# Kernel tuning notes

Measured on AMD Instinct MI355X. Metric: run time of the kernel, lower is better.

Reference implementation:

```python
import math
import jax, jax.numpy as jnp
import numpy as np

H = 1024          # hidden size
NH = 16           # num attention heads
HD = H // NH      # head dim = 64
MAXPOS = 1024
HYP_W = 0.5


def setup_inputs() -> dict:
    key = jax.random.key(0)
    ks = jax.random.split(key, 9)
    B, S = 4, 1024
    scale = 1.0 / math.sqrt(H)
    return {
        "hidden_states": jax.random.normal(ks[0], (B, S, H), jnp.float32),
        "attention_mask": jnp.zeros((B, 1, 1, S), jnp.float32),
        "hyperbolic_attention_scores": jax.random.normal(ks[1], (B, S, S), jnp.float32),
        "Wq": jax.random.normal(ks[2], (H, H), jnp.float32) * scale,
        "bq": jnp.zeros((H,), jnp.float32),
        "Wk": jax.random.normal(ks[3], (H, H), jnp.float32) * scale,
        "bk": jnp.zeros((H,), jnp.float32),
        "Wv": jax.random.normal(ks[4], (H, H), jnp.float32) * scale,
        "bv": jnp.zeros((H,), jnp.float32),
        "dist_emb": jax.random.normal(ks[5], (2 * MAXPOS - 1, HD), jnp.float32) * 0.02,
    }


def reference(hidden_states, attention_mask, hyperbolic_attention_scores,
              Wq, bq, Wk, bk, Wv, bv, dist_emb):
    B, S, _ = hidden_states.shape

    def split_heads(x):  # [B,S,H] -> [B,NH,S,HD]
        return x.reshape(B, S, NH, HD).transpose(0, 2, 1, 3)

    q = split_heads(hidden_states @ Wq + bq)
    k = split_heads(hidden_states @ Wk + bk)
    v = split_heads(hidden_states @ Wv + bv)

    # raw scores [B,NH,Sq,Sk]
    scores = jnp.einsum("bhqd,bhkd->bhqk", q, k)

    # relative_key_query position bias
    distance = jnp.arange(S)[:, None] - jnp.arange(S)[None, :]  # [Sq,Sk]
    pe = dist_emb[distance + MAXPOS - 1]                        # [Sq,Sk,HD]
    scores = scores + jnp.einsum("bhld,lrd->bhlr", q, pe)
    scores = scores + jnp.einsum("bhrd,lrd->bhlr", k, pe)

    scores = scores / math.sqrt(HD)
    scores = scores + HYP_W * hyperbolic_attention_scores[:, None, :, :]
    scores = scores + attention_mask

    probs = jax.nn.softmax(scores, axis=-1)
    ctx = jnp.einsum("bhqk,bhkd->bhqd", probs, v)  # [B,NH,S,HD]
    ctx = ctx.transpose(0, 2, 1, 3).reshape(B, S, H)
    return ctx
```

## Files before the change

kernel.cpp:

```cpp
#include <hip/hip_runtime.h>
#include <math.h>

#define S_SEQ 1024
#define NHEAD 16
#define HDIM  64
#define BATCH 4

typedef __attribute__((ext_vector_type(8))) short bf16x8;
typedef __attribute__((ext_vector_type(4))) float f32x4;

__device__ __forceinline__ float bf2f(unsigned short h) {
    union { unsigned u; float f; } un; un.u = ((unsigned)h) << 16; return un.f;
}
__device__ __forceinline__ unsigned short f2bf(float x) {
    union { float f; unsigned u; } un; un.f = x;
    unsigned r = un.u + 0x7FFFu + ((un.u >> 16) & 1u);
    return (unsigned short)(r >> 16);
}
__device__ __forceinline__ unsigned pack2bf(float a, float b) {
    return (unsigned)f2bf(a) | ((unsigned)f2bf(b) << 16);
}
__device__ __forceinline__ void glds16(const unsigned short* g, unsigned short* l) {
    __builtin_amdgcn_global_load_lds(
        (const __attribute__((address_space(1))) void*)g,
        (__attribute__((address_space(3))) void*)l, 16, 0, 0);
}

#define HS_F4 1048576
#define PE_F4 32752
__global__ __launch_bounds__(256) void conv_kernel(
    const float* __restrict__ hs, const float* __restrict__ de,
    unsigned short* __restrict__ hsb, unsigned short* __restrict__ peb)
{
    int i = blockIdx.x * 256 + threadIdx.x;
    if (i < HS_F4) {
        float4 v = ((const float4*)hs)[i];
        uint2 o;
        o.x = pack2bf(v.x, v.y);
        o.y = pack2bf(v.z, v.w);
        *(uint2*)(hsb + 4 * (size_t)i) = o;
    } else if (i < HS_F4 + PE_F4) {
        int j = i - HS_F4;
        float4 v = ((const float4*)de)[j];
        uint2 o;
        o.x = pack2bf(v.x, v.y);
        o.y = pack2bf(v.z, v.w);
        *(uint2*)(peb + 4 * (size_t)j) = o;
    }
}

__global__ __launch_bounds__(256) void wtrans_kernel(
    const float* __restrict__ Wq, const float* __restrict__ Wk,
    const float* __restrict__ Wv, unsigned short* __restrict__ wt)
{
    __shared__ float tl[64 * 67];
    const int which = blockIdx.z;
    const float* W = (which == 0) ? Wq : (which == 1) ? Wk : Wv;
    unsigned short* out = wt + (size_t)which * 1024 * 1024;
    const int k0 = blockIdx.x * 64, n0 = blockIdx.y * 64;
    const int t = threadIdx.x;

#pragma unroll
    for (int it = 0; it < 4; ++it) {
        int idx = t + it * 256;
        int kr = idx >> 4;
        int c4 = (idx & 15) << 2;
        float4 v = *(const float4*)(W + (size_t)(k0 + kr) * 1024 + n0 + c4);
        tl[kr * 67 + c4 + 0] = v.x; tl[kr * 67 + c4 + 1] = v.y;
        tl[kr * 67 + c4 + 2] = v.z; tl[kr * 67 + c4 + 3] = v.w;
    }
    __syncthreads();
#pragma unroll
    for (int it = 0; it < 2; ++it) {
        int idx = t + it * 256;
        int nr = idx >> 3;
        int k8 = (idx & 7) << 3;
        unsigned short r[8];
#pragma unroll
        for (int e = 0; e < 8; ++e) r[e] = f2bf(tl[(k8 + e) * 67 + nr]);
        uint4 o;
        o.x = (unsigned)r[0] | ((unsigned)r[1] << 16);
        o.y = (unsigned)r[2] | ((unsigned)r[3] << 16);
        o.z = (unsigned)r[4] | ((unsigned)r[5] << 16);
        o.w = (unsigned)r[6] | ((unsigned)r[7] << 16);
        *(uint4*)(out + (size_t)(n0 + nr) * 1024 + k0 + k8) = o;
    }
}

__global__ __launch_bounds__(256, 3) void qkv_mfma_kernel(
    const unsigned short* __restrict__ hsb, const unsigned short* __restrict__ wt,
    const float* __restrict__ bq, const float* __restrict__ bk,
    const float* __restrict__ bv,
    unsigned short* __restrict__ qo, unsigned short* __restrict__ ko,
    unsigned short* __restrict__ vo)
{
    __shared__ unsigned short As[128 * 64];
    __shared__ unsigned short Bs[128 * 64];

    const int t = threadIdx.x;
    const int lane = t & 63, w = t >> 6;
    const int l16 = lane & 15, quad = lane >> 4;
    const int wm = w >> 1, wn = w & 1;
    const int lrow = lane >> 3, cs = lane & 7;
    const int n0 = blockIdx.x * 128, m0 = blockIdx.y * 128;
    const int which = blockIdx.z;
    const unsigned short* wts = wt + (size_t)which * 1024 * 1024;
    const float* bias = (which == 0) ? bq : (which == 1) ? bk : bv;

    f32x4 acc[4][4];
#pragma unroll
    for (int i = 0; i < 4; ++i)
#pragma unroll
        for (int j = 0; j < 4; ++j) acc[i][j] = (f32x4){0.f, 0.f, 0.f, 0.f};

    for (int kk = 0; kk < 1024; kk += 64) {
#pragma unroll
        for (int it = 0; it < 4; ++it) {
            int mrow = 32 * w + 8 * it + lrow;
            int kch = cs ^ (mrow & 7);
            glds16(hsb + (size_t)(m0 + mrow) * 1024 + kk + kch * 8,
                   &As[(32 * w + 8 * it) * 64]);
            glds16(wts + (size_t)(n0 + mrow) * 1024 + kk + kch * 8,
                   &Bs[(32 * w + 8 * it) * 64]);
        }
        __syncthreads();

        bf16x8 af[4][2], bf[4][2];
#pragma unroll
        for (int i = 0; i < 4; ++i) {
            int am = 64 * wm + 16 * i + l16;
            int base = am * 64;
            af[i][0] = *(bf16x8*)&As[base + ((quad ^ (am & 7)) << 3)];
            af[i][1] = *(bf16x8*)&As[base + (((quad + 4) ^ (am & 7)) << 3)];
        }
#pragma unroll
        for (int j = 0; j < 4; ++j) {
            int bn = 64 * wn + 16 * j + l16;
            int base = bn * 64;
            bf[j][0] = *(bf16x8*)&Bs[base + ((quad ^ (bn & 7)) << 3)];
            bf[j][1] = *(bf16x8*)&Bs[base + (((quad + 4) ^ (bn & 7)) << 3)];
        }
#pragma unroll
        for (int i = 0; i < 4; ++i)
#pragma unroll
            for (int j = 0; j < 4; ++j) {
                acc[i][j] = __builtin_amdgcn_mfma_f32_16x16x32_bf16(
                    af[i][0], bf[j][0], acc[i][j], 0, 0, 0);
                acc[i][j] = __builtin_amdgcn_mfma_f32_16x16x32_bf16(
                    af[i][1], bf[j][1], acc[i][j], 0, 0, 0);
            }
        __syncthreads();
    }

#pragma unroll
    for (int j = 0; j < 4; ++j) {
        int n = n0 + 64 * wn + 16 * j + l16;
        float bvv = bias[n];
        int hh = n >> 6, hd = n & 63;
#pragma unroll
        for (int i = 0; i < 4; ++i) {
            int mb = m0 + 64 * wm + 16 * i + 4 * quad;
            int bb = mb >> 10, s = mb & 1023;
            if (which == 2) {
                uint2 o;
                o.x = pack2bf(acc[i][j][0] + bvv, acc[i][j][1] + bvv);
                o.y = pack2bf(acc[i][j][2] + bvv, acc[i][j][3] + bvv);
                *(uint2*)(vo + ((size_t)(bb * NHEAD + hh) * HDIM + hd) * S_SEQ + s) = o;
            } else {
                unsigned short* out = (which == 0) ? qo : ko;
#pragma unroll
                for (int r = 0; r < 4; ++r)
                    out[((size_t)(bb * NHEAD + hh) * S_SEQ + s + r) * HDIM + hd] =
                        f2bf(acc[i][j][r] + bvv);
            }
        }
    }
}

__global__ __launch_bounds__(256, 3) void attn_mfma_kernel(
    const unsigned short* __restrict__ qw, const unsigned short* __restrict__ kw,
    const unsigned short* __restrict__ vtw, const unsigned short* __restrict__ peb,
    const float* __restrict__ hyp, const float* __restrict__ mask,
    float* __restrict__ out)
{
    __shared__ unsigned short ks[32 * 72];
    __shared__ unsigned short vT[64 * 40];
    __shared__ unsigned short pes[96 * 72];
    __shared__ unsigned short QDs[96 * 66];
    __shared__ unsigned short KDs[96 * 38];
    __shared__ unsigned short ps[64 * 40];

    const int t = threadIdx.x;
    const int lane = t & 63, w = t >> 6;
    const int l16 = lane & 15, quad = lane >> 4;
    const int l0 = blockIdx.x * 64;
    const int h = blockIdx.y, b = blockIdx.z;

    const unsigned short* qb = qw + ((size_t)(b * NHEAD + h) * S_SEQ + l0) * HDIM;
    const unsigned short* kb = kw + (size_t)(b * NHEAD + h) * S_SEQ * HDIM;
    const unsigned short* vtb = vtw + (size_t)(b * NHEAD + h) * HDIM * S_SEQ;
    const float* hypb = hyp + (size_t)b * S_SEQ * S_SEQ;
    const float* maskb = mask + b * S_SEQ;

    const bf16x8 qf0 = *(const bf16x8*)(qb + (16 * w + l16) * 64 + quad * 8);
    const bf16x8 qf1 = *(const bf16x8*)(qb + (16 * w + l16) * 64 + 32 + quad * 8);

    const int pb0 = l0 + 992;

#pragma unroll
    for (int it = 0; it < 2; ++it) {
        int idx = t + it * 256;
        int row = idx >> 3, c8 = (idx & 7) << 3;
        int ar = pb0 + 32 + row;
        int slot = ar % 96;
        int src = ar > 2046 ? 2046 : ar;
        *(uint4*)&pes[slot * 72 + c8] = *(const uint4*)(peb + (size_t)src * 64 + c8);
    }
    __syncthreads();
#pragma unroll
    for (int jd = 0; jd < 4; ++jd) {
        int slot = (pb0 + 32 + 16 * jd + l16) % 96;
        bf16x8 p0 = *(bf16x8*)&pes[slot * 72 + quad * 8];
        bf16x8 p1 = *(bf16x8*)&pes[slot * 72 + 32 + quad * 8];
        f32x4 aq = (f32x4){0.f, 0.f, 0.f, 0.f};
        aq = __builtin_amdgcn_mfma_f32_16x16x32_bf16(qf0, p0, aq, 0, 0, 0);
        aq = __builtin_amdgcn_mfma_f32_16x16x32_bf16(qf1, p1, aq, 0, 0, 0);
        int ad = slot * 66 + 16 * w + 4 * quad;
        *(unsigned*)&QDs[ad] = pack2bf(aq[0], aq[1]);
        *(unsigned*)&QDs[ad + 2] = pack2bf(aq[2], aq[3]);
    }

    f32x4 accO[4];
#pragma unroll
    for (int j = 0; j < 4; ++j) accO[j] = (f32x4){0.f, 0.f, 0.f, 0.f};
    float m_run[4], lsum[4];
#pragma unroll
    for (int i = 0; i < 4; ++i) { m_run[i] = -INFINITY; lsum[i] = 0.f; }

    int sb = pb0 % 96;

    for (int kt = 0; kt < 32; ++kt) {
        const int r0 = 32 * kt;
        const int pb = pb0 - r0;

        {
            int row = t >> 3, c8 = (t & 7) << 3;
            *(uint4*)&ks[row * 72 + c8] =
                *(const uint4*)(kb + (size_t)(r0 + row) * 64 + c8);
            int d = t >> 2, rc = (t & 3) << 3;
            *(uint4*)&vT[d * 40 + rc] =
                *(const uint4*)(vtb + (size_t)d * 1024 + r0 + rc);
            int slot = sb + row; if (slot >= 96) slot -= 96;
            *(uint4*)&pes[slot * 72 + c8] =
                *(const uint4*)(peb + (size_t)(pb + row) * 64 + c8);
        }
        __syncthreads();

        bf16x8 kfA0 = *(bf16x8*)&ks[(16 * (w & 1) + l16) * 72 + quad * 8];
        bf16x8 kfA1 = *(bf16x8*)&ks[(16 * (w & 1) + l16) * 72 + 32 + quad * 8];
        f32x4 accS[2];
#pragma unroll
        for (int j = 0; j < 2; ++j) {
            bf16x8 b0 = *(bf16x8*)&ks[(16 * j + l16) * 72 + quad * 8];
            bf16x8 b1 = *(bf16x8*)&ks[(16 * j + l16) * 72 + 32 + quad * 8];
            f32x4 a = (f32x4){0.f, 0.f, 0.f, 0.f};
            a = __builtin_amdgcn_mfma_f32_16x16x32_bf16(qf0, b0, a, 0, 0, 0);
            a = __builtin_amdgcn_mfma_f32_16x16x32_bf16(qf1, b1, a, 0, 0, 0);
            accS[j] = a;
        }
#pragma unroll
        for (int jd = 0; jd < 2; ++jd) {
            int slot = sb + 16 * jd + l16; if (slot >= 96) slot -= 96;
            bf16x8 p0 = *(bf16x8*)&pes[slot * 72 + quad * 8];
            bf16x8 p1 = *(bf16x8*)&pes[slot * 72 + 32 + quad * 8];
            f32x4 aq = (f32x4){0.f, 0.f, 0.f, 0.f};
            aq = __builtin_amdgcn_mfma_f32_16x16x32_bf16(qf0, p0, aq, 0, 0, 0);
            aq = __builtin_amdgcn_mfma_f32_16x16x32_bf16(qf1, p1, aq, 0, 0, 0);
            int ad = slot * 66 + 16 * w + 4 * quad;
            *(unsigned*)&QDs[ad] = pack2bf(aq[0], aq[1]);
            *(unsigned*)&QDs[ad + 2] = pack2bf(aq[2], aq[3]);
        }
#pragma unroll
        for (int jk = 0; jk < 3; ++jk) {
            int dd = 48 * (w >> 1) + 16 * jk + l16;
            int slot = sb + dd; if (slot >= 96) slot -= 96;
            bf16x8 p0 = *(bf16x8*)&pes[slot * 72 + quad * 8];
            bf16x8 p1 = *(bf16x8*)&pes[slot * 72 + 32 + quad * 8];
            f32x4 ak = (f32x4){0.f, 0.f, 0.f, 0.f};
            ak = __builtin_amdgcn_mfma_f32_16x16x32_bf16(kfA0, p0, ak, 0, 0, 0);
            ak = __builtin_amdgcn_mfma_f32_16x16x32_bf16(kfA1, p1, ak, 0, 0, 0);
            int ad = dd * 38 + 16 * (w & 1) + 4 * quad;
            *(unsigned*)&KDs[ad] = pack2bf(ak[0], ak[1]);
            *(unsigned*)&KDs[ad + 2] = pack2bf(ak[2], ak[3]);
        }
        __syncthreads();

        float sc[4][2], al[4];
#pragma unroll
        for (int j = 0; j < 2; ++j) {
            int r_loc = 16 * j + l16;
            float mv = maskb[r0 + r_loc];
#pragma unroll
            for (int i = 0; i < 4; ++i) {
                int ll = 16 * w + 4 * quad + i;
                int di = ll - r_loc + 31;
                int sl = sb + di; if (sl >= 96) sl -= 96;
                float qd = bf2f(QDs[sl * 66 + ll]);
                float kd = bf2f(KDs[di * 38 + r_loc]);
                float hv = hypb[(size_t)(l0 + ll) * 1024 + r0 + r_loc];
                sc[i][j] = (accS[j][i] + qd + kd) * 0.125f + 0.5f * hv + mv;
            }
        }
#pragma unroll
        for (int i = 0; i < 4; ++i) {
            float mx = fmaxf(sc[i][0], sc[i][1]);
#pragma unroll
            for (int off = 1; off < 16; off <<= 1)
                mx = fmaxf(mx, __shfl_xor(mx, off));
            float m_new = fmaxf(m_run[i], mx);
            al[i] = __expf(m_run[i] - m_new);
            float p0 = __expf(sc[i][0] - m_new);
            float p1 = __expf(sc[i][1] - m_new);
            sc[i][0] = p0; sc[i][1] = p1;
            float rs = p0 + p1;
#pragma unroll
            for (int off = 1; off < 16; off <<= 1)
                rs += __shfl_xor(rs, off);
            lsum[i] = lsum[i] * al[i] + rs;
            m_run[i] = m_new;
        }
#pragma unroll
        for (int i = 0; i < 4; ++i) {
            int ll = 16 * w + 4 * quad + i;
            ps[ll * 40 + l16] = f2bf(sc[i][0]);
            ps[ll * 40 + 16 + l16] = f2bf(sc[i][1]);
        }

        bf16x8 pf = *(bf16x8*)&ps[(16 * w + l16) * 40 + quad * 8];
#pragma unroll
        for (int jf = 0; jf < 4; ++jf) {
            bf16x8 vv = *(bf16x8*)&vT[(16 * jf + l16) * 40 + quad * 8];
            f32x4 o = accO[jf];
#pragma unroll
            for (int r = 0; r < 4; ++r) o[r] *= al[r];
            o = __builtin_amdgcn_mfma_f32_16x16x32_bf16(pf, vv, o, 0, 0, 0);
            accO[jf] = o;
        }
        sb -= 32; if (sb < 0) sb += 96;
        __syncthreads();
    }

#pragma unroll
    for (int jf = 0; jf < 4; ++jf)
#pragma unroll
        for (int i = 0; i < 4; ++i) {
            int ll = 16 * w + 4 * quad + i;
            out[((size_t)b * S_SEQ + l0 + ll) * 1024 + h * 64 + 16 * jf + l16] =
                accO[jf][i] / lsum[i];
        }
}

extern "C" void kernel_launch(void* const* d_in, const int* in_sizes, int n_in,
                              void* d_out, int out_size, void* d_ws, size_t ws_size,
                              hipStream_t stream) {
    const float* hs   = (const float*)d_in[0];
    const float* mask = (const float*)d_in[1];
    const float* hyp  = (const float*)d_in[2];
    const float* Wq   = (const float*)d_in[3];
    const float* bq   = (const float*)d_in[4];
    const float* Wk   = (const float*)d_in[5];
    const float* bk   = (const float*)d_in[6];
    const float* Wv   = (const float*)d_in[7];
    const float* bv   = (const float*)d_in[8];
    const float* de   = (const float*)d_in[9];

    char* ws = (char*)d_ws;
    unsigned short* qw  = (unsigned short*)(ws);
    unsigned short* kw  = (unsigned short*)(ws + (8u << 20));
    unsigned short* vtw = (unsigned short*)(ws + (16u << 20));
    unsigned short* hsb = (unsigned short*)(ws + (24u << 20));
    unsigned short* wt  = (unsigned short*)(ws + (32u << 20));
    unsigned short* peb = (unsigned short*)(ws + (38u << 20));

    conv_kernel<<<dim3((HS_F4 + PE_F4 + 255) / 256), 256, 0, stream>>>(hs, de, hsb, peb);
    wtrans_kernel<<<dim3(16, 16, 3), 256, 0, stream>>>(Wq, Wk, Wv, wt);
    qkv_mfma_kernel<<<dim3(8, 32, 3), 256, 0, stream>>>(hsb, wt, bq, bk, bv, qw, kw, vtw);
    attn_mfma_kernel<<<dim3(16, NHEAD, BATCH), 256, 0, stream>>>(
        qw, kw, vtw, peb, hyp, mask, (float*)d_out);
}
```

Measured before the change: 286.9 us.

## Widen attention key tiles to 64 with direct-to-LDS loads and 32x32 MFMA position bias

The attention kernel now processes 64 keys per iteration instead of 32. It loads K, V^T and the relative-position embedding tiles straight into XOR-swizzled LDS with global_load_lds, and computes the query and key position-bias products with 32x32x16 MFMAs. The grid is reordered so heads sharing a batch's hyperbolic-score rows are scheduled adjacently, and the probability tile reuses the K buffer. The aim is fewer barriers and loop iterations per key, less bank conflict and better cache reuse, at the cost of more LDS and registers, with occupancy lowered to 2 blocks per CU.

Result: slower. 315.6 us (+10.0%).

```diff
diff --git a/kernel.cpp b/kernel.cpp
--- a/kernel.cpp
+++ b/kernel.cpp
@@ -8,6 +8,7 @@
 
 typedef __attribute__((ext_vector_type(8))) short bf16x8;
 typedef __attribute__((ext_vector_type(4))) float f32x4;
+typedef __attribute__((ext_vector_type(16))) float f32x16;
 
 __device__ __forceinline__ float bf2f(unsigned short h) {
     union { unsigned u; float f; } un; un.u = ((unsigned)h) << 16; return un.f;
@@ -177,24 +178,24 @@
     }
 }
 
-__global__ __launch_bounds__(256, 3) void attn_mfma_kernel(
+__global__ __launch_bounds__(256, 2) void attn_mfma_kernel(
     const unsigned short* __restrict__ qw, const unsigned short* __restrict__ kw,
     const unsigned short* __restrict__ vtw, const unsigned short* __restrict__ peb,
     const float* __restrict__ hyp, const float* __restrict__ mask,
     float* __restrict__ out)
 {
-    __shared__ unsigned short ks[32 * 72];
-    __shared__ unsigned short vT[64 * 40];
-    __shared__ unsigned short pes[96 * 72];
-    __shared__ unsigned short QDs[96 * 66];
-    __shared__ unsigned short KDs[96 * 38];
-    __shared__ unsigned short ps[64 * 40];
+    __shared__ unsigned short ks[64 * 64];
+    __shared__ unsigned short vT[64 * 64];
+    __shared__ unsigned short pes[128 * 64];
+    __shared__ unsigned short QDs[64 * 132];
+    __shared__ unsigned short KDs[64 * 132];
 
     const int t = threadIdx.x;
     const int lane = t & 63, w = t >> 6;
     const int l16 = lane & 15, quad = lane >> 4;
-    const int l0 = blockIdx.x * 64;
-    const int h = blockIdx.y, b = blockIdx.z;
+    const int l32 = lane & 31, h5 = lane >> 5;
+    const int cs8 = lane & 7, r8 = lane >> 3;
+    const int h = blockIdx.x, l0 = blockIdx.y * 64, b = blockIdx.z;
 
     const unsigned short* qb = qw + ((size_t)(b * NHEAD + h) * S_SEQ + l0) * HDIM;
     const unsigned short* kb = kw + (size_t)(b * NHEAD + h) * S_SEQ * HDIM;
@@ -202,32 +203,50 @@
     const float* hypb = hyp + (size_t)b * S_SEQ * S_SEQ;
     const float* maskb = mask + b * S_SEQ;
 
-    const bf16x8 qf0 = *(const bf16x8*)(qb + (16 * w + l16) * 64 + quad * 8);
-    const bf16x8 qf1 = *(const bf16x8*)(qb + (16 * w + l16) * 64 + 32 + quad * 8);
-
-    const int pb0 = l0 + 992;
-
-#pragma unroll
-    for (int it = 0; it < 2; ++it) {
-        int idx = t + it * 256;
-        int row = idx >> 3, c8 = (idx & 7) << 3;
-        int ar = pb0 + 32 + row;
-        int slot = ar % 96;
-        int src = ar > 2046 ? 2046 : ar;
-        *(uint4*)&pes[slot * 72 + c8] = *(const uint4*)(peb + (size_t)src * 64 + c8);
+    const bf16x8 qfA0 = *(const bf16x8*)(qb + (16 * w + l16) * 64 + quad * 8);
+    const bf16x8 qfA1 = *(const bf16x8*)(qb + (16 * w + l16) * 64 + 32 + quad * 8);
+    bf16x8 qB[2][4];
+#pragma unroll
+    for (int lg = 0; lg < 2; ++lg)
+#pragma unroll
+        for (int f = 0; f < 4; ++f)
+            qB[lg][f] = *(const bf16x8*)(qb + (32 * lg + l32) * 64 + 16 * f + 8 * h5);
+
+    const int A0 = l0 + 960;
+    int sbase = A0 & 127;
+
+    {
+        int pslot = (sbase + 64) & 127;
+#pragma unroll
+        for (int it = 0; it < 2; ++it) {
+            int off = 16 * w + 8 * it + r8;
+            int absr = A0 + 64 + off; if (absr > 2046) absr = 2046;
+            glds16(peb + (size_t)absr * 64 + ((cs8 ^ (off & 7)) << 3),
+                   &pes[(pslot + 16 * w + 8 * it) * 64]);
+        }
     }
     __syncthreads();
-#pragma unroll
-    for (int jd = 0; jd < 4; ++jd) {
-        int slot = (pb0 + 32 + 16 * jd + l16) % 96;
-        bf16x8 p0 = *(bf16x8*)&pes[slot * 72 + quad * 8];
-        bf16x8 p1 = *(bf16x8*)&pes[slot * 72 + 32 + quad * 8];
-        f32x4 aq = (f32x4){0.f, 0.f, 0.f, 0.f};
-        aq = __builtin_amdgcn_mfma_f32_16x16x32_bf16(qf0, p0, aq, 0, 0, 0);
-        aq = __builtin_amdgcn_mfma_f32_16x16x32_bf16(qf1, p1, aq, 0, 0, 0);
-        int ad = slot * 66 + 16 * w + 4 * quad;
-        *(unsigned*)&QDs[ad] = pack2bf(aq[0], aq[1]);
-        *(unsigned*)&QDs[ad + 2] = pack2bf(aq[2], aq[3]);
+    {
+        int ddg = 2 + (w >> 1), lg = w & 1;
+        f32x16 aQ;
+#pragma unroll
+        for (int e = 0; e < 16; ++e) aQ[e] = 0.f;
+        int srow = (sbase + 32 * ddg + l32) & 127;
+#pragma unroll
+        for (int f = 0; f < 4; ++f) {
+            int ch = 2 * f + h5;
+            bf16x8 pA = *(bf16x8*)&pes[srow * 64 + ((ch ^ (srow & 7)) << 3)];
+            aQ = __builtin_amdgcn_mfma_f32_32x32x16_bf16(pA, qB[lg][f], aQ, 0, 0, 0);
+        }
+        int colL = 32 * lg + l32;
+#pragma unroll
+        for (int q_ = 0; q_ < 4; ++q_) {
+            int slot0 = (sbase + 32 * ddg + 8 * q_ + 4 * h5) & 127;
+            uint2 o;
+            o.x = pack2bf(aQ[4 * q_ + 0], aQ[4 * q_ + 1]);
+            o.y = pack2bf(aQ[4 * q_ + 2], aQ[4 * q_ + 3]);
+            *(uint2*)&QDs[colL * 132 + slot0] = o;
+        }
     }
 
     f32x4 accO[4];
@@ -237,117 +256,168 @@
 #pragma unroll
     for (int i = 0; i < 4; ++i) { m_run[i] = -INFINITY; lsum[i] = 0.f; }
 
-    int sb = pb0 % 96;
-
-    for (int kt = 0; kt < 32; ++kt) {
-        const int r0 = 32 * kt;
-        const int pb = pb0 - r0;
-
+    for (int kt = 0; kt < 16; ++kt) {
+        const int r0 = 64 * kt;
+        const int pbase = A0 - r0;
+        __syncthreads();
+
+#pragma unroll
+        for (int it = 0; it < 2; ++it) {
+            int row = 16 * w + 8 * it + r8;
+            glds16(kb + (size_t)(r0 + row) * 64 + ((cs8 ^ (row & 7)) << 3),
+                   &ks[(16 * w + 8 * it) * 64]);
+            glds16(vtb + (size_t)row * 1024 + r0 + ((cs8 ^ (row & 7)) << 3),
+                   &vT[(16 * w + 8 * it) * 64]);
+            glds16(peb + (size_t)(pbase + row) * 64 + ((cs8 ^ (row & 7)) << 3),
+                   &pes[(sbase + 16 * w + 8 * it) * 64]);
+        }
+        __syncthreads();
+
+        float hv[4][4], mv[4];
+#pragma unroll
+        for (int j = 0; j < 4; ++j) {
+            mv[j] = maskb[r0 + 16 * j + l16];
+#pragma unroll
+            for (int i = 0; i < 4; ++i)
+                hv[i][j] = hypb[(size_t)(l0 + 16 * w + 4 * quad + i) * 1024 +
+                                r0 + 16 * j + l16];
+        }
+
+        f32x4 accS[4];
+#pragma unroll
+        for (int j = 0; j < 4; ++j) {
+            int row = 16 * j + l16;
+            bf16x8 b0 = *(bf16x8*)&ks[row * 64 + ((quad ^ (row & 7)) << 3)];
+            bf16x8 b1 = *(bf16x8*)&ks[row * 64 + (((quad + 4) ^ (row & 7)) << 3)];
+            f32x4 a = (f32x4){0.f, 0.f, 0.f, 0.f};
+            a = __builtin_amdgcn_mfma_f32_16x16x32_bf16(qfA0, b0, a, 0, 0, 0);
+            a = __builtin_amdgcn_mfma_f32_16x16x32_bf16(qfA1, b1, a, 0, 0, 0);
+            accS[j] = a;
+        }
         {
-            int row = t >> 3, c8 = (t & 7) << 3;
-            *(uint4*)&ks[row * 72 + c8] =
-                *(const uint4*)(kb + (size_t)(r0 + row) * 64 + c8);
-            int d = t >> 2, rc = (t & 3) << 3;
-            *(uint4*)&vT[d * 40 + rc] =
-                *(const uint4*)(vtb + (size_t)d * 1024 + r0 + rc);
-            int slot = sb + row; if (slot >= 96) slot -= 96;
-            *(uint4*)&pes[slot * 72 + c8] =
-                *(const uint4*)(peb + (size_t)(pb + row) * 64 + c8);
+            int rg = w >> 1;
+            int rrow = 32 * rg + l32;
+            bf16x8 kB[4];
+#pragma unroll
+            for (int f = 0; f < 4; ++f) {
+                int ch = 2 * f + h5;
+                kB[f] = *(bf16x8*)&ks[rrow * 64 + ((ch ^ (rrow & 7)) << 3)];
+            }
+#pragma unroll
+            for (int dt = 0; dt < 2; ++dt) {
+                int dig = 2 * (w & 1) + dt;
+                f32x16 aK;
+#pragma unroll
+                for (int e = 0; e < 16; ++e) aK[e] = 0.f;
+                int srow = (sbase + 32 * dig + l32) & 127;
+#pragma unroll
+                for (int f = 0; f < 4; ++f) {
+                    int ch = 2 * f + h5;
+                    bf16x8 pA = *(bf16x8*)&pes[srow * 64 + ((ch ^ (srow & 7)) << 3)];
+                    aK = __builtin_amdgcn_mfma_f32_32x32x16_bf16(pA, kB[f], aK, 0, 0, 0);
+                }
+#pragma unroll
+                for (int q_ = 0; q_ < 4; ++q_) {
+                    int di0 = 32 * dig + 8 * q_ + 4 * h5;
+                    uint2 o;
+                    o.x = pack2bf(aK[4 * q_ + 0], aK[4 * q_ + 1]);
+                    o.y = pack2bf(aK[4 * q_ + 2], aK[4 * q_ + 3]);
+                    *(uint2*)&KDs[rrow * 132 + di0] = o;
+                }
+            }
+        }
+        {
+            int ddg = w >> 1, lg = w & 1;
+            f32x16 aQ;
+#pragma unroll
+            for (int e = 0; e < 16; ++e) aQ[e] = 0.f;
+            int srow = (sbase + 32 * ddg + l32) & 127;
+#pragma unroll
+            for (int f = 0; f < 4; ++f) {
+                int ch = 2 * f + h5;
+                bf16x8 pA = *(bf16x8*)&pes[srow * 64 + ((ch ^ (srow & 7)) << 3)];
+                aQ = __builtin_amdgcn_mfma_f32_32x32x16_bf16(pA, qB[lg][f], aQ, 0, 0, 0);
+            }
+            int colL = 32 * lg + l32;
+#pragma unroll
+            for (int q_ = 0; q_ < 4; ++q_) {
+                int slot0 = (sbase + 32 * ddg + 8 * q_ + 4 * h5) & 127;
+                uint2 o;
+                o.x = pack2bf(aQ[4 * q_ + 0], aQ[4 * q_ + 1]);
+                o.y = pack2bf(aQ[4 * q_ + 2], aQ[4 * q_ + 3]);
+                *(uint2*)&QDs[colL * 132 + slot0] = o;
+            }
         }
         __syncthreads();
 
-        bf16x8 kfA0 = *(bf16x8*)&ks[(16 * (w & 1) + l16) * 72 + quad * 8];
-        bf16x8 kfA1 = *(bf16x8*)&ks[(16 * (w & 1) + l16) * 72 + 32 + quad * 8];
-        f32x4 accS[2];
-#pragma unroll
-        for (int j = 0; j < 2; ++j) {
-            bf16x8 b0 = *(bf16x8*)&ks[(16 * j + l16) * 72 + quad * 8];
-            bf16x8 b1 = *(bf16x8*)&ks[(16 * j + l16) * 72 + 32 + quad * 8];
-            f32x4 a = (f32x4){0.f, 0.f, 0.f, 0.f};
-            a = __builtin_amdgcn_mfma_f32_16x16x32_bf16(qf0, b0, a, 0, 0, 0);
-            a = __builtin_amdgcn_mfma_f32_16x16x32_bf16(qf1, b1, a, 0, 0, 0);
-            accS[j] = a;
-        }
-#pragma unroll
-        for (int jd = 0; jd < 2; ++jd) {
-            int slot = sb + 16 * jd + l16; if (slot >= 96) slot -= 96;
-            bf16x8 p0 = *(bf16x8*)&pes[slot * 72 + quad * 8];
-            bf16x8 p1 = *(bf16x8*)&pes[slot * 72 + 32 + quad * 8];
-            f32x4 aq = (f32x4){0.f, 0.f, 0.f, 0.f};
-            aq = __builtin_amdgcn_mfma_f32_16x16x32_bf16(qf0, p0, aq, 0, 0, 0);
-            aq = __builtin_amdgcn_mfma_f32_16x16x32_bf16(qf1, p1, aq, 0, 0, 0);
-            int ad = slot * 66 + 16 * w + 4 * quad;
-            *(unsigned*)&QDs[ad] = pack2bf(aq[0], aq[1]);
-            *(unsigned*)&QDs[ad + 2] = pack2bf(aq[2], aq[3]);
-        }
-#pragma unroll
-        for (int jk = 0; jk < 3; ++jk) {
-            int dd = 48 * (w >> 1) + 16 * jk + l16;
-            int slot = sb + dd; if (slot >= 96) slot -= 96;
-            bf16x8 p0 = *(bf16x8*)&pes[slot * 72 + quad * 8];
-            bf16x8 p1 = *(bf16x8*)&pes[slot * 72 + 32 + quad * 8];
-            f32x4 ak = (f32x4){0.f, 0.f, 0.f, 0.f};
-            ak = __builtin_amdgcn_mfma_f32_16x16x32_bf16(kfA0, p0, ak, 0, 0, 0);
-            ak = __builtin_amdgcn_mfma_f32_16x16x32_bf16(kfA1, p1, ak, 0, 0, 0);
-            int ad = dd * 38 + 16 * (w & 1) + 4 * quad;
-            *(unsigned*)&KDs[ad] = pack2bf(ak[0], ak[1]);
-            *(unsigned*)&KDs[ad + 2] = pack2bf(ak[2], ak[3]);
-        }
-        __syncthreads();
-
-        float sc[4][2], al[4];
-#pragma unroll
-        for (int j = 0; j < 2; ++j) {
+        float sc[4][4], al[4];
+#pragma unroll
+        for (int j = 0; j < 4; ++j) {
             int r_loc = 16 * j + l16;
-            float mv = maskb[r0 + r_loc];
 #pragma unroll
             for (int i = 0; i < 4; ++i) {
                 int ll = 16 * w + 4 * quad + i;
-                int di = ll - r_loc + 31;
-                int sl = sb + di; if (sl >= 96) sl -= 96;
-                float qd = bf2f(QDs[sl * 66 + ll]);
-                float kd = bf2f(KDs[di * 38 + r_loc]);
-                float hv = hypb[(size_t)(l0 + ll) * 1024 + r0 + r_loc];
-                sc[i][j] = (accS[j][i] + qd + kd) * 0.125f + 0.5f * hv + mv;
+                int di = ll - r_loc + 63;
+                int slot = (sbase + di) & 127;
+                float qd = bf2f(QDs[ll * 132 + slot]);
+                float kd = bf2f(KDs[r_loc * 132 + di]);
+                sc[i][j] = (accS[j][i] + qd + kd) * 0.125f + 0.5f * hv[i][j] + mv[j];
             }
         }
 #pragma unroll
         for (int i = 0; i < 4; ++i) {
-            float mx = fmaxf(sc[i][0], sc[i][1]);
+            float mx = fmaxf(fmaxf(sc[i][0], sc[i][1]), fmaxf(sc[i][2], sc[i][3]));
 #pragma unroll
             for (int off = 1; off < 16; off <<= 1)
                 mx = fmaxf(mx, __shfl_xor(mx, off));
             float m_new = fmaxf(m_run[i], mx);
             al[i] = __expf(m_run[i] - m_new);
-            float p0 = __expf(sc[i][0] - m_new);
-            float p1 = __expf(sc[i][1] - m_new);
-            sc[i][0] = p0; sc[i][1] = p1;
-            float rs = p0 + p1;
+            float rs = 0.f;
+#pragma unroll
+            for (int j = 0; j < 4; ++j) {
+                float p = __expf(sc[i][j] - m_new);
+                sc[i][j] = p;
+                rs += p;
+            }
 #pragma unroll
             for (int off = 1; off < 16; off <<= 1)
                 rs += __shfl_xor(rs, off);
             lsum[i] = lsum[i] * al[i] + rs;
             m_run[i] = m_new;
         }
-#pragma unroll
-        for (int i = 0; i < 4; ++i) {
-            int ll = 16 * w + 4 * quad + i;
-            ps[ll * 40 + l16] = f2bf(sc[i][0]);
-            ps[ll * 40 + 16 + l16] = f2bf(sc[i][1]);
-        }
-
-        bf16x8 pf = *(bf16x8*)&ps[(16 * w + l16) * 40 + quad * 8];
-#pragma unroll
-        for (int jf = 0; jf < 4; ++jf) {
-            bf16x8 vv = *(bf16x8*)&vT[(16 * jf + l16) * 40 + quad * 8];
-            f32x4 o = accO[jf];
-#pragma unroll
-            for (int r = 0; r < 4; ++r) o[r] *= al[r];
-            o = __builtin_amdgcn_mfma_f32_16x16x32_bf16(pf, vv, o, 0, 0, 0);
-            accO[jf] = o;
-        }
-        sb -= 32; if (sb < 0) sb += 96;
-        __syncthreads();
+        {
+            unsigned short* ps = ks;
+#pragma unroll
+            for (int i = 0; i < 4; ++i) {
+                int ll = 16 * w + 4 * quad + i;
+#pragma unroll
+                for (int j = 0; j < 4; ++j) {
+                    int r_loc = 16 * j + l16;
+                    ps[ll * 64 + (((r_loc >> 3) ^ (ll & 7)) << 3) + (r_loc & 7)] =
+                        f2bf(sc[i][j]);
+                }
+            }
+        }
+
+        {
+            const unsigned short* ps = ks;
+            int prow = 16 * w + l16;
+            bf16x8 pf0 = *(bf16x8*)&ps[prow * 64 + ((quad ^ (prow & 7)) << 3)];
+            bf16x8 pf1 = *(bf16x8*)&ps[prow * 64 + (((quad + 4) ^ (prow & 7)) << 3)];
+#pragma unroll
+            for (int jf = 0; jf < 4; ++jf) {
+                int vrow = 16 * jf + l16;
+                bf16x8 v0 = *(bf16x8*)&vT[vrow * 64 + ((quad ^ (vrow & 7)) << 3)];
+                bf16x8 v1 = *(bf16x8*)&vT[vrow * 64 + (((quad + 4) ^ (vrow & 7)) << 3)];
+                f32x4 o = accO[jf];
+#pragma unroll
+                for (int r = 0; r < 4; ++r) o[r] *= al[r];
+                o = __builtin_amdgcn_mfma_f32_16x16x32_bf16(pf0, v0, o, 0, 0, 0);
+                o = __builtin_amdgcn_mfma_f32_16x16x32_bf16(pf1, v1, o, 0, 0, 0);
+                accO[jf] = o;
+            }
+        }
+        sbase = (sbase + 64) & 127;
     }
 
 #pragma unroll
@@ -385,6 +455,6 @@
     conv_kernel<<<dim3((HS_F4 + PE_F4 + 255) / 256), 256, 0, stream>>>(hs, de, hsb, peb);
     wtrans_kernel<<<dim3(16, 16, 3), 256, 0, stream>>>(Wq, Wk, Wv, wt);
     qkv_mfma_kernel<<<dim3(8, 32, 3), 256, 0, stream>>>(hsb, wt, bq, bk, bv, qw, kw, vtw);
-    attn_mfma_kernel<<<dim3(16, NHEAD, BATCH), 256, 0, stream>>>(
+    attn_mfma_kernel<<<dim3(NHEAD, S_SEQ / 64, BATCH), 256, 0, stream>>>(
         qw, kw, vtw, peb, hyp, mask, (float*)d_out);
 }
```
